# Kernel optimization log

Hardware: AMD Instinct MI355X
Metric: run time of the kernel (lower is better)

## Reference

```python
import jax, jax.numpy as jnp
import numpy as np

H = W = 256
L = H * W                      # number of graph vertices / tree leaves
N_NODES = 2 * L - 1            # binary partition tree node count
LAM = 1.0                      # lambda_ (soft-area temperature)


def _grid_edges():
    """4-adjacency grid graph edges (same structure as higra get_4_adjacency_graph)."""
    idx = np.arange(L, dtype=np.int64).reshape(H, W)
    src = np.concatenate([idx[:, :-1].ravel(), idx[:-1, :].ravel()])
    dst = np.concatenate([idx[:, 1:].ravel(), idx[1:, :].ravel()])
    return src.astype(np.int32), dst.astype(np.int32)


def setup_inputs() -> dict:
    key = jax.random.key(0)
    src, dst = _grid_edges()
    ew = jax.random.uniform(key, (src.shape[0],), dtype=jnp.float32)
    return {"edge_weights": ew,
            "edges_src": jnp.asarray(src),
            "edges_dst": jnp.asarray(dst)}


def _build_tree(ew, src, dst):
    """higra.bpt_canonical: Kruskal over stably-sorted edges, building a binary
    merge tree. Leaves are 0..L-1, internal node L+i is created by the i-th MST
    edge. Returns (sizes, mst_edge_map, ancestor paths). All integer structure
    is piecewise-constant w.r.t. edge_weights (no gradient flows through it)."""
    order = np.argsort(ew, kind="stable")
    uf = np.arange(L)

    def find(x):
        r = x
        while uf[r] != r:
            r = uf[r]
        while uf[x] != r:
            uf[x], x = r, uf[x]
        return r

    canon = np.arange(L)                      # tree node of each union-find root
    parent = np.arange(N_NODES)               # self-parent until set (root keeps self)
    sizes = np.ones(N_NODES, dtype=np.float32)
    edge_map = np.zeros(L - 1, dtype=np.int64)
    node = L
    for ei in order:
        a = find(src[ei]); b = find(dst[ei])
        if a == b:
            continue
        na, nb = canon[a], canon[b]
        parent[na] = node
        parent[nb] = node
        sizes[node] = sizes[na] + sizes[nb]
        edge_map[node - L] = ei
        uf[a] = b
        canon[b] = node
        node += 1
    # self-inclusive ancestor paths, padded by repeating the root
    cur = np.arange(N_NODES)
    cols = [cur.copy()]
    while np.any(parent[cur] != cur):
        cur = parent[cur]
        cols.append(cur.copy())
    paths = np.stack(cols, axis=1)            # [N_NODES, D+1]
    return sizes, edge_map, paths


def _softarea(edge_weights, edge_map, sizes_np, paths_np):
    """Soft area of every tree node n:
       area(n) = sum_x sigmoid((alt(n) - d(x, n)) / lambda)
    where d(x,n) is the min ultrametric distance from leaf x to the leaves of n:
      - x in subtree(n), x != n : d = alt(parent(x))
      - x == n (leaf)           : d = 0
      - x outside subtree(n)    : d = alt(lowest ancestor of n containing x).
    Outside leaves are grouped per ancestor a (count = size(a) - size(previous
    node on the path)), giving an O(N * depth) vectorized computation."""
    alt = jnp.concatenate([jnp.zeros((L,), edge_weights.dtype),
                           edge_weights[edge_map]])          # [N_NODES]
    alt_path = alt[paths_np]                                  # [N, D+1]
    size_path = sizes_np[paths_np]                            # constant, numpy
    diff = jnp.asarray(size_path[:, 1:] - size_path[:, :-1])  # 0 on root padding
    outside = jnp.sum(
        diff * jax.nn.sigmoid((alt[:, None] - alt_path[:, 1:]) / LAM), axis=1)

    # inside: each leaf x contributes sigmoid((alt(a_k) - alt(parent(x)))/lam)
    # to every proper ancestor a_k, plus sigmoid(0)=0.5 to itself (alt(leaf)=0).
    lp = paths_np[:L]                                         # [L, D+1]
    alt_lp = alt_path[:L]
    valid = jnp.asarray((lp[:, 1:] != lp[:, :-1]).astype(np.float32))
    vals = jax.nn.sigmoid((alt_lp[:, 1:] - alt_lp[:, 1:2]) / LAM) * valid
    inside = jax.ops.segment_sum(vals.reshape(-1),
                                 jnp.asarray(lp[:, 1:].reshape(-1)),
                                 num_segments=N_NODES)
    inside = inside.at[:L].add(0.5)
    return inside + outside


def reference(edge_weights, edges_src, edges_dst):
    sizes, edge_map, paths = _build_tree(np.asarray(edge_weights),
                                         np.asarray(edges_src),
                                         np.asarray(edges_dst))
    return _softarea(edge_weights, jnp.asarray(edge_map), sizes, paths)
```

## Files before the change

kernel.cpp:

```cpp
#include <hip/hip_runtime.h>
#include <stdint.h>

typedef unsigned int u32;
typedef unsigned short u16;
typedef unsigned long long u64;

#define L_VERTS 65536
#define N_EDGES 130560
#define N_NODES 131071
#define NODEPAD 131072

#define CCH 170
#define CCHM 86
#define SCH 768
#define PADM (CCHM*SCH)
#define NMST (L_VERTS-1)
#define MAXSV 1536
#define HSZ 2048

#define NB 255
#define TPB 64
#define IPT 8
#define IPB 512

__global__ void init_keys(const float* __restrict__ w, u32* __restrict__ keys, u32* __restrict__ vals,
                          u32* szG, u16* canonTop16, u32* parent, float* alt){
  int i = blockIdx.x*blockDim.x + threadIdx.x;
  if(i < N_EDGES){ keys[i] = __float_as_uint(w[i]); vals[i] = (u32)i; }
  if(i < N_NODES){ parent[i]=(u32)i; alt[i]=0.f; }
  if(i < L_VERTS){ szG[i]=1u; canonTop16[i]=0xFFFFu; }
}

__global__ void radix_hist(const u32* __restrict__ idx, const u32* __restrict__ keys,
                           u32* __restrict__ histG, int shift){
  __shared__ u32 h[256];
  for(int i=threadIdx.x;i<256;i+=TPB) h[i]=0;
  __syncthreads();
  int base = blockIdx.x*IPB + threadIdx.x*IPT;
  #pragma unroll
  for(int i=0;i<IPT;i++){
    u32 e = idx[base+i];
    u32 d = (keys[e]>>shift)&255u;
    atomicAdd(&h[d],1u);
  }
  __syncthreads();
  for(int i=threadIdx.x;i<256;i+=TPB) histG[i*NB+blockIdx.x]=h[i];
}

__global__ void radix_scan(u32* histG){
  const int M = 256*NB;
  __shared__ u32 sums[1024];
  int t=threadIdx.x; int s=t*64; u32 acc=0;
  for(int i=0;i<64;i++){int id=s+i; if(id<M) acc+=histG[id];}
  sums[t]=acc; __syncthreads();
  for(int off=1; off<1024; off<<=1){
    u32 v=(t>=off)?sums[t-off]:0u;
    __syncthreads();
    sums[t]+=v;
    __syncthreads();
  }
  u32 run = (t==0)?0u:sums[t-1];
  for(int i=0;i<64;i++){int id=s+i; if(id<M){u32 v=histG[id]; histG[id]=run; run+=v;}}
}

__global__ void radix_scatter(const u32* __restrict__ idxIn, const u32* __restrict__ keys,
                              u32* __restrict__ idxOut, const u32* __restrict__ histG, int shift){
  __shared__ u16 thoff[256][TPB];
  int t=threadIdx.x;
  for(int d=t;d<256;d+=TPB) for(int j=0;j<TPB;j++) thoff[d][j]=0;
  __syncthreads();
  int base = blockIdx.x*IPB + t*IPT;
  u32 myv[IPT]; u32 myd[IPT];
  #pragma unroll
  for(int i=0;i<IPT;i++){
    myv[i]=idxIn[base+i];
    myd[i]=(keys[myv[i]]>>shift)&255u;
    thoff[myd[i]][t]++;
  }
  __syncthreads();
  for(int dd=0;dd<4;dd++){
    int d=t*4+dd; u32 run=0;
    for(int j=0;j<TPB;j++){ u32 v=thoff[d][j]; thoff[d][j]=(u16)run; run+=v; }
  }
  __syncthreads();
  #pragma unroll
  for(int i=0;i<IPT;i++){
    u32 d=myd[i];
    u32 pos = histG[d*NB+blockIdx.x] + (u32)thoff[d][t];
    thoff[d][t]++;
    idxOut[pos]=myv[i];
  }
}

__global__ void build_epair(const u32* __restrict__ order, const int* __restrict__ srcv,
                            const int* __restrict__ dstv, u32* __restrict__ epair){
  int p=blockIdx.x*blockDim.x+threadIdx.x;
  if(p>=N_EDGES) return;
  u32 e=order[p];
  epair[p]=((u32)dstv[e]<<16)|(u32)srcv[e];
}

#define CBK 255
#define CT 512

__device__ __forceinline__ u32 bfind(const u32* __restrict__ parentB, u32 x){
  while(true){ u32 p=parentB[x]; if(p==x) return x; x=p; }
}

__global__ void bor_init(u32* parentB, u32* minE, unsigned char* mstF){
  int i=blockIdx.x*blockDim.x+threadIdx.x;
  if(i<L_VERTS){ parentB[i]=(u32)i; minE[i]=0xFFFFFFFFu; }
  if(i<N_EDGES) mstF[i]=0;
}

__global__ void bor_minedge(const u32* __restrict__ epair, const u32* __restrict__ parentB,
                            u32* __restrict__ minE){
  int p=blockIdx.x*blockDim.x+threadIdx.x;
  u32 pr=epair[p];
  u32 ra=bfind(parentB, pr&0xFFFFu), rb=bfind(parentB, pr>>16);
  if(ra==rb) return;
  atomicMin(&minE[ra],(u32)p);
  atomicMin(&minE[rb],(u32)p);
}

__global__ void bor_hookA(const u32* __restrict__ epair, const u32* __restrict__ parentB,
                          const u32* __restrict__ minE, u32* __restrict__ nextB,
                          unsigned char* __restrict__ mstF){
  int v=blockIdx.x*blockDim.x+threadIdx.x;
  if(v>=L_VERTS) return;
  if(parentB[v]!=(u32)v) return;
  u32 p=minE[v];
  if(p==0xFFFFFFFFu) return;
  u32 pr=epair[p];
  u32 ra=bfind(parentB, pr&0xFFFFu), rb=bfind(parentB, pr>>16);
  u32 w2=(ra==(u32)v)?rb:ra;
  nextB[v]=w2;
  mstF[p]=1;
}

__global__ void bor_hookB(u32* __restrict__ parentB, const u32* __restrict__ minE,
                          const u32* __restrict__ nextB){
  int v=blockIdx.x*blockDim.x+threadIdx.x;
  if(v>=L_VERTS) return;
  if(parentB[v]!=(u32)v) return;
  u32 p=minE[v];
  if(p==0xFFFFFFFFu) return;
  u32 w2=nextB[v];
  if(minE[w2]==p && (u32)v<w2) return;
  parentB[v]=w2;
}

__global__ void bor_compress(u32* __restrict__ parentB, u32* __restrict__ minE){
  int v=blockIdx.x*blockDim.x+threadIdx.x;
  if(v>=L_VERTS) return;
  u32 x=(u32)v;
  while(true){ u32 px=parentB[x]; if(px==x) break; u32 g=parentB[px]; if(g!=px) parentB[x]=g; x=g; }
  parentB[v]=x;
  minE[v]=0xFFFFFFFFu;
}

__global__ void mst_count(const unsigned char* __restrict__ mstF, u32* __restrict__ blockCnt){
  int b=blockIdx.x, t=threadIdx.x;
  int p=b*CT+t;
  u64 m=__ballot(mstF[p]!=0);
  __shared__ u32 ws[8];
  if((t&63)==0) ws[t>>6]=(u32)__popcll(m);
  __syncthreads();
  if(t==0){ u32 s=0; for(int i=0;i<8;i++) s+=ws[i]; blockCnt[b]=s; }
}

__global__ void mst_scan(const u32* __restrict__ blockCnt, u32* __restrict__ blockBase,
                         u32* __restrict__ mepair){
  int t=threadIdx.x;
  __shared__ u32 s[256];
  u32 v=(t<CBK)?blockCnt[t]:0u;
  s[t]=v; __syncthreads();
  for(int o=1;o<256;o<<=1){ u32 x=(t>=o)?s[t-o]:0u; __syncthreads(); s[t]+=x; __syncthreads(); }
  if(t<CBK) blockBase[t]=s[t]-v;
  u32 total=s[255];
  for(u32 j=total+(u32)t; j<(u32)PADM; j+=256u) mepair[j]=0u;
}

__global__ void mst_scatter(const unsigned char* __restrict__ mstF, const u32* __restrict__ blockBase,
                            const u32* __restrict__ order, const u32* __restrict__ epair,
                            u32* __restrict__ morder, u32* __restrict__ mepair){
  int b=blockIdx.x, t=threadIdx.x;
  int p=b*CT+t;
  u32 f=(u32)mstF[p];
  u64 m=__ballot(f!=0);
  __shared__ u32 ws[8];
  int wid=t>>6, lane=t&63;
  if(lane==0) ws[wid]=(u32)__popcll(m);
  __syncthreads();
  if(t==0){ u32 s2=0; for(int i=0;i<8;i++){ u32 x=ws[i]; ws[i]=s2; s2+=x; } }
  __syncthreads();
  if(f){
    u32 pre=(u32)__popcll(m & ((1ull<<lane)-1ull));
    u32 pos=blockBase[b]+ws[wid]+pre;
    morder[pos]=order[p];
    mepair[pos]=epair[p];
  }
}

__device__ __forceinline__ u32 ald(u32* p){
  return __hip_atomic_load(p, __ATOMIC_RELAXED, __HIP_MEMORY_SCOPE_AGENT);
}
__device__ __forceinline__ void ast(u32* p, u32 v){
  __hip_atomic_store(p, v, __ATOMIC_RELAXED, __HIP_MEMORY_SCOPE_AGENT);
}

__global__ void __launch_bounds__(1024,1) p1_checkpoints(
    const u32* __restrict__ epair,
    u32* szG, u16* lid16, u16* svroot16, u16* svsize16, u16* svnext16, u32* mG)
{
  __shared__ u16 ufL[L_VERTS];
  __shared__ u32 hkey[HSZ];
  __shared__ u32 sufL[MAXSV];
  __shared__ u32 compsz[MAXSV];
  __shared__ u32 repkey[MAXSV];
  __shared__ u16 lidL[2*SCH];
  __shared__ u32 mcnt;
  int t = threadIdx.x;
  for(int i=t;i<L_VERTS/2;i+=1024) ((u32*)ufL)[i]=((2u*(u32)i+1u)<<16)|(2u*(u32)i);
  for(int k=0;k<CCHM;k++){
    for(int i=t;i<HSZ;i+=1024) hkey[i]=0xFFFFFFFFu;
    for(u32 s=t;s<MAXSV;s+=1024){ sufL[s]=s; compsz[s]=0u; repkey[s]=0u; }
    if(t==0) mcnt=0u;
    __syncthreads();
    int base = k*SCH;
    for(int i=t;i<2*SCH;i+=1024){
      u32 pr = epair[base+(i>>1)];
      u32 v = (i&1)? (pr>>16) : (pr&0xFFFFu);
      u32 x=v;
      while(true){ u32 px=ufL[x]; if(px==x)break; u32 g=ufL[px]; if(g!=px) ufL[x]=(u16)g; x=g; }
      u32 r=x;
      if(v!=r) ufL[v]=(u16)r;
      u32 h=(r*2654435761u)>>21;
      while(true){
        u32 old=atomicCAS(&hkey[h],0xFFFFFFFFu,(r<<16)|0x7FFFu);
        if(old==0xFFFFFFFFu){
          u32 id=atomicAdd(&mcnt,1u);
          svroot16[k*MAXSV+id]=(u16)r;
          hkey[h]=(r<<16)|id;
          break;
        }
        if((old>>16)==r) break;
        h=(h+1)&(HSZ-1u);
      }
      lidL[i]=(u16)h;
    }
    __syncthreads();
    u32 mc=mcnt;
    if(t==0) mG[k]=mc;
    for(u32 s=t;s<mc;s+=1024){
      u32 r=(u32)svroot16[k*MAXSV+s];
      svsize16[k*MAXSV+s]=(u16)(ald(&szG[r])-1u);
    }
    for(int i=t;i<2*SCH;i+=1024) lid16[2*base+i]=(u16)(hkey[lidL[i]]&0xFFFFu);
    for(int j=t;j<SCH;j+=1024){
      u32 sa=hkey[lidL[2*j]]&0xFFFFu, sb=hkey[lidL[2*j+1]]&0xFFFFu;
      if(sa==sb) continue;
      while(true){
        u32 x=sa; while(true){u32 p2=sufL[x]; if(p2==x)break; u32 g=sufL[p2]; if(g!=p2) sufL[x]=g; x=g;}
        u32 y=sb; while(true){u32 p2=sufL[y]; if(p2==y)break; u32 g=sufL[p2]; if(g!=p2) sufL[y]=g; y=g;}
        if(x==y) break;
        u32 hi=x>y?x:y, lo=x^y^hi;
        if(atomicCAS(&sufL[hi],hi,lo)==hi) break;
        sa=hi; sb=lo;
      }
    }
    __syncthreads();
    for(u32 s=t;s<mc;s+=1024){
      u32 x=s; while(true){u32 p2=sufL[x]; if(p2==x)break; x=p2;}
      sufL[s]=x;
      u32 sz=(u32)svsize16[k*MAXSV+s]+1u;
      atomicAdd(&compsz[x], sz);
      atomicMax(&repkey[x], (sz<<11) | (2047u-s));
    }
    __syncthreads();
    for(u32 s=t;s<mc;s+=1024){
      u32 rs=sufL[s];
      u32 rep=2047u-(repkey[rs]&2047u);
      u32 wv=(u32)svroot16[k*MAXSV+rep];
      svnext16[k*MAXSV+s]=(u16)wv;
      u32 myroot=(u32)svroot16[k*MAXSV+s];
      if(myroot!=wv) ufL[myroot]=(u16)wv;
      if(s==rep)     ast(&szG[wv], compsz[rs]);
    }
    __syncthreads();
  }
}

__global__ void __launch_bounds__(64) p2_chunk(
  const u16* __restrict__ lid16,
  const u16* __restrict__ svsize16, const u16* __restrict__ svnext16, const u32* __restrict__ mG,
  u16* __restrict__ outChA, u16* __restrict__ outChB, u16* __restrict__ outSize16, u16* __restrict__ outJ16,
  u32* __restrict__ accCnt, u16* __restrict__ compR16, u16* __restrict__ compTop16, u32* __restrict__ ncomp)
{
  int k = blockIdx.x; int t = threadIdx.x;
  __shared__ u16 uf[MAXSV];
  __shared__ u32 csize[MAXSV];
  __shared__ u16 ctop[MAXSV];
  __shared__ u16 svnl[MAXSV];
  __shared__ u32 lidP[SCH];
  __shared__ u32 cmp_s;
  u32 m = mG[k];
  int base=k*SCH;
  for(u32 s=t;s<m;s+=64){
    uf[s]=(u16)s;
    csize[s]=(u32)svsize16[k*MAXSV+s]+1u;
    ctop[s]=(u16)s;
    svnl[s]=svnext16[k*MAXSV+s];
  }
  for(int j=t;j<SCH;j+=64) lidP[j]=((const u32*)lid16)[base+j];
  if(t==0) cmp_s=0u;
  __syncthreads();
  if(t==0){
    u32 cnt=0;
    for(int j=0;j<SCH;j++){
      u32 lw = lidP[j];
      u32 la = lw & 0xFFFFu, lb = lw >> 16;
      u32 x=la; while(true){u32 px=uf[x]; if(px==x)break; u32 g=uf[px]; uf[x]=(u16)g; x=g;}
      u32 y=lb; while(true){u32 py=uf[y]; if(py==y)break; u32 g=uf[py]; uf[y]=(u16)g; y=g;}
      if(x==y) continue;
      u32 sa=csize[x], sb=csize[y], ns=sa+sb;
      outChA[base+cnt]=ctop[x];
      outChB[base+cnt]=ctop[y];
      outSize16[base+cnt]=(u16)(ns-1u);
      outJ16[base+cnt]=(u16)j;
      u32 win=(sa>=sb)?x:y, los=x^y^win;
      uf[los]=(u16)win; csize[win]=ns; ctop[win]=(u16)(0x8000u|cnt);
      cnt++;
    }
    accCnt[k]=cnt;
  }
  __syncthreads();
  for(u32 s=t;s<m;s+=64){
    if(uf[s]==(u16)s && (ctop[s]&0x8000u)){
      u32 pos=atomicAdd(&cmp_s,1u);
      compR16[k*MAXSV+pos]=svnl[s];
      compTop16[k*MAXSV+pos]=(u16)(ctop[s]&0x7FFFu);
    }
  }
  __syncthreads();
  if(t==0) ncomp[k]=cmp_s;
}

__global__ void __launch_bounds__(1024) p3_stitch(
  const u32* __restrict__ accCnt, const u16* __restrict__ outChA, const u16* __restrict__ outChB,
  const u16* __restrict__ outSize16, const u16* __restrict__ outJ16,
  const u16* __restrict__ svroot16,
  const u16* __restrict__ compR16, const u16* __restrict__ compTop16, const u32* __restrict__ ncomp,
  const u32* __restrict__ morder, const float* __restrict__ w,
  u16* __restrict__ canonTop16, u32* __restrict__ parent, float* __restrict__ alt, u16* __restrict__ usize16)
{
  __shared__ u32 accBase[CCH];
  int t=threadIdx.x;
  if(t==0){ u32 r=0; for(int k=0;k<CCHM;k++){ accBase[k]=r; r+=accCnt[k]; } }
  __syncthreads();
  for(int idx=t; idx<PADM; idx+=1024){
    int k = idx/SCH; int j = idx - k*SCH;
    if(j < (int)accCnt[k]){
      u32 nid = (u32)L_VERTS + accBase[k] + (u32)j;
      u32 p = (u32)(k*SCH) + (u32)outJ16[idx];
      alt[nid] = w[morder[p]];
      usize16[nid] = outSize16[idx];
      u32 cA=outChA[idx]; if(cA & 0x8000u) parent[(u32)L_VERTS+accBase[k]+(cA&0x7FFFu)] = nid;
      u32 cB=outChB[idx]; if(cB & 0x8000u) parent[(u32)L_VERTS+accBase[k]+(cB&0x7FFFu)] = nid;
    }
  }
  __syncthreads();
  for(int k=0;k<CCHM;k++){
    u32 ac=accCnt[k];
    for(u32 j=t;j<ac;j+=1024){
      u32 idx=(u32)(k*SCH)+j;
      u32 nid=(u32)L_VERTS+accBase[k]+j;
      u32 cA=outChA[idx];
      if(!(cA&0x8000u)){
        u32 root=(u32)svroot16[k*MAXSV+cA];
        u32 ct=(u32)canonTop16[root];
        parent[(ct==0xFFFFu)?root:((u32)L_VERTS+ct)]=nid;
      }
      u32 cB=outChB[idx];
      if(!(cB&0x8000u)){
        u32 root=(u32)svroot16[k*MAXSV+cB];
        u32 ct=(u32)canonTop16[root];
        parent[(ct==0xFFFFu)?root:((u32)L_VERTS+ct)]=nid;
      }
    }
    __syncthreads();
    u32 nc=ncomp[k];
    for(u32 j=t;j<nc;j+=1024){
      canonTop16[(u32)compR16[k*MAXSV+j]] = (u16)(accBase[k]+compTop16[k*MAXSV+j]);
    }
    __syncthreads();
  }
}

__device__ __forceinline__ void hvals6(float v, float* o){
  float v2=v*v, v3=v2*v, v4=v2*v2, v5=v4*v;
  o[0]=0.5f-0.25f*v+v3*(1.f/48.f)-v5*(1.f/480.f);
  o[1]=0.25f-v2*(1.f/16.f)+v4*(1.f/96.f);
  o[2]=v*(1.f/16.f)-v3*(1.f/48.f);
  o[3]=v2*(1.f/48.f)-(1.f/48.f);
  o[4]=-v*(1.f/96.f);
  o[5]=(1.f/480.f);
}

__global__ void zero_both(u32* cc, float* nodeM, u32* ctr){
  int i=blockIdx.x*blockDim.x+threadIdx.x;
  if(i<L_VERTS) cc[i]=0u;
  if(i<6*NODEPAD) nodeM[i]=0.f;
  if(i==0) *ctr=0u;
}

__global__ void prep_init(const u32* __restrict__ parent, const u16* __restrict__ usize16,
                          u32* cc, u32* J0, uint2* A0, float* out){
  int n=blockIdx.x*blockDim.x+threadIdx.x;
  if(n>=N_NODES) return;
  out[n] = (n<L_VERTS)?0.5f:0.0f;
  if(n==N_NODES-1){ J0[n]=(u32)n; A0[n]=make_uint2(0u,0u); return; }
  u32 p=parent[n];
  u32 ord=atomicAdd(&cc[p-L_VERTS],1u);
  u32 szP=(u32)usize16[p]+1u;
  u32 szN=(n<L_VERTS)?1u:((u32)usize16[n]+1u);
  u32 sib=szP-szN;
  A0[n]=make_uint2(ord? sib:0u, 1u + (ord? (2u*sib-1u):0u));
  J0[n]=p;
}

__global__ void triple_round(const u32* __restrict__ Jin, const uint2* __restrict__ Ain,
                             u32* __restrict__ Jout, uint2* __restrict__ Aout){
  int n=blockIdx.x*blockDim.x+threadIdx.x;
  if(n>=N_NODES) return;
  u32 j1=Jin[n], j2=Jin[j1], j3=Jin[j2], j4=Jin[j3], j5=Jin[j4], j6=Jin[j5], j7=Jin[j6];
  uint2 a0=Ain[n], a1=Ain[j1], a2=Ain[j2], a3=Ain[j3], a4=Ain[j4], a5=Ain[j5], a6=Ain[j6], a7=Ain[j7];
  Aout[n]=make_uint2(a0.x+a1.x+a2.x+a3.x+a4.x+a5.x+a6.x+a7.x,
                     a0.y+a1.y+a2.y+a3.y+a4.y+a5.y+a6.y+a7.y);
  Jout[n]=Jin[j7];
}

__global__ void scatter_all(const u32* __restrict__ parent, const float* __restrict__ alt,
                            const u16* __restrict__ usize16, const uint2* __restrict__ accF,
                            float* __restrict__ leafM, float* __restrict__ nodeM){
  int n=blockIdx.x*blockDim.x+threadIdx.x;
  if(n>=N_NODES) return;
  u32 p=parent[n];
  float h[6]; hvals6(alt[p],h);
  uint2 af=accF[n];
  if(n<L_VERTS){
    u32 pos=af.x;
    #pragma unroll
    for(int j=0;j<6;j++) leafM[(size_t)j*L_VERTS+pos]=h[j];
  }
  if(n<N_NODES-1){
    u32 szP=(u32)usize16[p]+1u;
    u32 szN=(n<L_VERTS)?1u:((u32)usize16[n]+1u);
    float d=(float)(szP-szN);
    u32 q0=af.y;
    u32 q1=q0 + 2u*szN - 1u;
    #pragma unroll
    for(int j=0;j<6;j++){
      float tm=d*h[j];
      atomicAdd(&nodeM[(size_t)j*NODEPAD+q0], tm);
      atomicAdd(&nodeM[(size_t)j*NODEPAD+q1], -tm);
    }
  }
}

__global__ void scanAll(float* __restrict__ leafM, float* __restrict__ nodeM,
                        float* __restrict__ bsumL, float* __restrict__ bsumN, u32* ctr){
  int b=blockIdx.x; int t=threadIdx.x;
  float* arr; u32 base; float* bs;
  if(b<6*64){ int row=b>>6, blk=b&63;  arr=leafM+(size_t)row*L_VERTS;  base=(u32)blk*1024u; bs=&bsumL[row*64+blk]; }
  else      { int bb=b-384; int row=bb>>7, blk=bb&127; arr=nodeM+(size_t)row*NODEPAD; base=(u32)blk*1024u; bs=&bsumN[row*128+blk]; }
  __shared__ float s[256];
  __shared__ u32 lastFlag;
  base += (u32)t*4u;
  float v0=arr[base],v1=arr[base+1],v2=arr[base+2],v3=arr[base+3];
  v1+=v0; v2+=v1; v3+=v2;
  s[t]=v3; __syncthreads();
  for(int o=1;o<256;o<<=1){ float x=(t>=o)?s[t-o]:0.f; __syncthreads(); s[t]+=x; __syncthreads(); }
  float pre=(t>0)?s[t-1]:0.f;
  arr[base]=v0+pre; arr[base+1]=v1+pre; arr[base+2]=v2+pre; arr[base+3]=v3+pre;
  if(t==255) *bs=s[255];
  __threadfence();
  if(t==0) lastFlag = (atomicAdd(ctr,1u)==1151u) ? 1u : 0u;
  __syncthreads();
  if(lastFlag){
    __threadfence();
    if(t<6){ float r=0; for(int i=0;i<64;i++){ float v=bsumL[t*64+i]; bsumL[t*64+i]=r; r+=v; } }
    else if(t<12){ int j=t-6; float r=0; for(int i=0;i<128;i++){ float v=bsumN[j*128+i]; bsumN[j*128+i]=r; r+=v; } }
  }
}

__global__ void eval_all(const uint2* __restrict__ accF, const float* __restrict__ alt,
                         const u16* __restrict__ usize16, const float* __restrict__ leafM,
                         const float* __restrict__ nodeM, const float* __restrict__ bsumL,
                         const float* __restrict__ bsumN, float* __restrict__ out){
  int n=blockIdx.x*blockDim.x+threadIdx.x;
  if(n>=N_NODES) return;
  uint2 af=accF[n];
  float u=alt[n];
  u32 q=af.y;
  float acc=0.f, up=1.f;
  #pragma unroll
  for(int j=0;j<6;j++){
    float T = nodeM[(size_t)j*NODEPAD+q] + bsumN[j*128 + (q>>10)];
    acc += up*T;
    up*=u;
  }
  if(n>=L_VERTS){
    u32 lo=af.x;
    u32 hi=lo + (u32)usize16[n] + 1u;
    up=1.f;
    #pragma unroll
    for(int j=0;j<6;j++){
      const float* arr=leafM + (size_t)j*L_VERTS;
      const float* bs=bsumL + j*64;
      float Ph = arr[hi-1u] + bs[(hi-1u)>>10];
      float Pl = lo ? (arr[lo-1u] + bs[(lo-1u)>>10]) : 0.f;
      acc += up*(Ph-Pl);
      up*=u;
    }
  }
  out[n]+=acc;
}

__global__ void ws_too_small(float* out){
  int i=blockIdx.x*blockDim.x+threadIdx.x;
  if(i<N_NODES) out[i]=1.0e6f;
}

extern "C" void kernel_launch(void* const* d_in, const int* in_sizes, int n_in,
                              void* d_out, int out_size, void* d_ws, size_t ws_size,
                              hipStream_t stream){
  (void)in_sizes; (void)n_in; (void)out_size;
  const float* w  = (const float*)d_in[0];
  const int* src  = (const int*)d_in[1];
  const int* dst  = (const int*)d_in[2];
  float* out = (float*)d_out;

  char* ws = (char*)d_ws;
  size_t off=0;
  auto alloc=[&](size_t bytes)->void*{ void* p = ws+off; off += (bytes+511)&~(size_t)511; return p; };
  u32* parent   =(u32*)alloc((size_t)N_NODES*4);
  float* alt    =(float*)alloc((size_t)N_NODES*4);
  u16* usize16  =(u16*)alloc((size_t)N_NODES*2);
  float* bsumL  =(float*)alloc(6*64*4);
  float* bsumN  =(float*)alloc(6*128*4);
  u32* ctr      =(u32*)alloc(512);
  size_t scratch0=off;
  u32* keys0    =(u32*)alloc((size_t)N_EDGES*4);
  u32* vals0    =(u32*)alloc((size_t)N_EDGES*4);
  u32* vals1    =(u32*)alloc((size_t)N_EDGES*4);
  u32* histG    =(u32*)alloc(256*NB*4);
  u16* canonTop16=(u16*)alloc((size_t)L_VERTS*2);
  u16* outJ16   =(u16*)alloc((size_t)N_EDGES*2);
  u16* svroot16 =(u16*)alloc((size_t)CCH*MAXSV*2);
  u16* svsize16 =(u16*)alloc((size_t)CCH*MAXSV*2);
  u16* svnext16 =(u16*)alloc((size_t)CCH*MAXSV*2);
  u32* mG       =(u32*)alloc(CCH*4);
  u32* accCnt   =(u32*)alloc(CCH*4);
  u32* ncomp    =(u32*)alloc(CCH*4);
  u32* parentB  =(u32*)alloc((size_t)L_VERTS*4);
  u32* minE     =(u32*)alloc((size_t)L_VERTS*4);
  u32* nextB    =(u32*)alloc((size_t)L_VERTS*4);
  unsigned char* mstF=(unsigned char*)alloc((size_t)N_EDGES);
  u32* blockCnt =(u32*)alloc(256*4);
  u32* blockBase=(u32*)alloc(256*4);
  u32* morder   =(u32*)alloc((size_t)PADM*4);
  u32* mepair   =(u32*)alloc((size_t)PADM*4);
  size_t endA=off;
  off=scratch0;
  u32* ccChsum  =(u32*)alloc((size_t)L_VERTS*4);
  u32* J0       =(u32*)alloc((size_t)N_NODES*4);
  u32* J1       =(u32*)alloc((size_t)N_NODES*4);
  uint2* A0     =(uint2*)alloc((size_t)N_NODES*8);
  uint2* A1     =(uint2*)alloc((size_t)N_NODES*8);
  float* nodeM  =(float*)alloc((size_t)6*NODEPAD*4);
  size_t endB=off;
  float* leafM  =(float*)ccChsum;

  if((endA>ws_size)||(endB>ws_size)){
    ws_too_small<<<(N_NODES+255)/256,256,0,stream>>>(out);
    return;
  }

  u16* lid16    =(u16*)vals1;
  u32* epair    =keys0;
  u16* outChA16 =(u16*)histG;
  u16* outChB16 =(u16*)keys0;
  u16* outSize16=(u16*)((char*)keys0 + (size_t)N_EDGES*2);
  u16* compR16  =svsize16;
  u16* compTop16=svnext16;
  u32* szG      =(u32*)usize16;

  init_keys<<<(N_NODES+255)/256,256,0,stream>>>(w,keys0,vals0,szG,canonTop16,parent,alt);
  for(int pass=0;pass<4;pass++){
    const u32* iv = (pass&1)?vals1:vals0;
    u32* ov = (pass&1)?vals0:vals1;
    int shift=pass*8;
    radix_hist   <<<NB,TPB,0,stream>>>(iv,keys0,histG,shift);
    radix_scan   <<<1,1024,0,stream>>>(histG);
    radix_scatter<<<NB,TPB,0,stream>>>(iv,keys0,ov,histG,shift);
  }
  build_epair<<<(N_EDGES+255)/256,256,0,stream>>>(vals0,src,dst,epair);
  bor_init<<<CBK,CT,0,stream>>>(parentB,minE,mstF);
  for(int r=0;r<16;r++){
    bor_minedge <<<CBK,CT,0,stream>>>(epair,parentB,minE);
    bor_hookA   <<<L_VERTS/CT,CT,0,stream>>>(epair,parentB,minE,nextB,mstF);
    bor_hookB   <<<L_VERTS/CT,CT,0,stream>>>(parentB,minE,nextB);
    bor_compress<<<L_VERTS/CT,CT,0,stream>>>(parentB,minE);
  }
  mst_count  <<<CBK,CT,0,stream>>>(mstF,blockCnt);
  mst_scan   <<<1,256,0,stream>>>(blockCnt,blockBase,mepair);
  mst_scatter<<<CBK,CT,0,stream>>>(mstF,blockBase,vals0,epair,morder,mepair);
  p1_checkpoints<<<1,1024,0,stream>>>(mepair,szG,lid16,svroot16,svsize16,svnext16,mG);
  p2_chunk<<<CCHM,64,0,stream>>>(lid16,svsize16,svnext16,mG,
                                outChA16,outChB16,outSize16,outJ16,accCnt,compR16,compTop16,ncomp);
  p3_stitch<<<1,1024,0,stream>>>(accCnt,outChA16,outChB16,outSize16,outJ16,svroot16,
                                 compR16,compTop16,ncomp,morder,w,canonTop16,parent,alt,usize16);
  zero_both<<<(6*NODEPAD+255)/256,256,0,stream>>>(ccChsum,nodeM,ctr);
  prep_init<<<(N_NODES+255)/256,256,0,stream>>>(parent,usize16,ccChsum,J1,A1,out);
  for(int r=0;r<6;r++){
    if((r&1)==0) triple_round<<<(N_NODES+255)/256,256,0,stream>>>(J1,A1,J0,A0);
    else         triple_round<<<(N_NODES+255)/256,256,0,stream>>>(J0,A0,J1,A1);
  }
  const uint2* accF=A1;
  scatter_all<<<(N_NODES+255)/256,256,0,stream>>>(parent,alt,usize16,accF,leafM,nodeM);
  scanAll<<<1152,256,0,stream>>>(leafM,nodeM,bsumL,bsumN,ctr);
  eval_all<<<(N_NODES+255)/256,256,0,stream>>>(accF,alt,usize16,leafM,nodeM,bsumL,bsumN,out);
}
```

Before: 2.699 ms.

## Fuse Boruvka MST rounds into one cooperative kernel with early exit

Replaces the 64 separate Boruvka kernel launches (init plus 16 rounds of four phases) with a single cooperative kernel that uses grid-wide syncs between phases. A hook counter ends the loop early once all MST edges are found, and edges whose endpoints already share a component are marked dead so later rounds skip their finds. Separately, the single-block checkpoint kernel now reads component sizes while inserting into the hash table. It also picks the union-find root as the representative instead of the largest component, which removes an atomicMax and a pass over the supervertices. The cost is grid-sync overhead, and the representative choice is a possible semantic change.

Result: slower. 3.755 ms (+39.1%).

```diff
diff --git a/kernel.cpp b/kernel.cpp
--- a/kernel.cpp
+++ b/kernel.cpp
@@ -1,5 +1,8 @@
 #include <hip/hip_runtime.h>
+#include <hip/hip_cooperative_groups.h>
 #include <stdint.h>
+
+namespace cg = cooperative_groups;
 
 typedef unsigned int u32;
 typedef unsigned short u16;
@@ -100,64 +103,68 @@
   epair[p]=((u32)dstv[e]<<16)|(u32)srcv[e];
 }
 
+#define BORB 256
+#define BORT 512
+#define DEADE 0xFFFFFFFFu
+
+__device__ __forceinline__ u32 bfind(const u32* __restrict__ parentB, u32 x){
+  while(true){ u32 p=parentB[x]; if(p==x) return x; x=p; }
+}
+
+__global__ void __launch_bounds__(BORT) bor_all(u32* __restrict__ epair, u32* __restrict__ parentB,
+                        u32* __restrict__ minE, u32* __restrict__ nextB,
+                        unsigned char* __restrict__ mstF, u32* __restrict__ bctr){
+  cg::grid_group grid = cg::this_grid();
+  int tid = blockIdx.x*BORT + threadIdx.x;
+  if(tid<L_VERTS){ parentB[tid]=(u32)tid; minE[tid]=0xFFFFFFFFu; }
+  if(tid<N_EDGES) mstF[tid]=0;
+  if(tid==0) bctr[0]=0u;
+  grid.sync();
+  for(int r=0;r<16;r++){
+    if(tid<N_EDGES){
+      u32 pr=epair[tid];
+      if(pr!=DEADE){
+        u32 ra=bfind(parentB, pr&0xFFFFu), rb=bfind(parentB, pr>>16);
+        if(ra==rb){ if(!mstF[tid]) epair[tid]=DEADE; }
+        else { atomicMin(&minE[ra],(u32)tid); atomicMin(&minE[rb],(u32)tid); }
+      }
+    }
+    grid.sync();
+    if(tid<L_VERTS && parentB[tid]==(u32)tid){
+      u32 p=minE[tid];
+      if(p!=0xFFFFFFFFu){
+        u32 pr=epair[p];
+        u32 ra=bfind(parentB, pr&0xFFFFu), rb=bfind(parentB, pr>>16);
+        u32 w2=(ra==(u32)tid)?rb:ra;
+        nextB[tid]=w2;
+        mstF[p]=1;
+      }
+    }
+    grid.sync();
+    if(tid<L_VERTS && parentB[tid]==(u32)tid){
+      u32 p=minE[tid];
+      if(p!=0xFFFFFFFFu){
+        u32 w2=nextB[tid];
+        if(!(minE[w2]==p && (u32)tid<w2)){
+          parentB[tid]=w2;
+          atomicAdd(&bctr[0],1u);
+        }
+      }
+    }
+    grid.sync();
+    if(tid<L_VERTS){
+      u32 x=(u32)tid;
+      while(true){ u32 px=parentB[x]; if(px==x) break; u32 g=parentB[px]; if(g!=px) parentB[x]=g; x=g; }
+      parentB[tid]=x;
+      minE[tid]=0xFFFFFFFFu;
+    }
+    grid.sync();
+    if(__hip_atomic_load(&bctr[0], __ATOMIC_RELAXED, __HIP_MEMORY_SCOPE_AGENT) >= (u32)NMST) break;
+  }
+}
+
 #define CBK 255
 #define CT 512
-
-__device__ __forceinline__ u32 bfind(const u32* __restrict__ parentB, u32 x){
-  while(true){ u32 p=parentB[x]; if(p==x) return x; x=p; }
-}
-
-__global__ void bor_init(u32* parentB, u32* minE, unsigned char* mstF){
-  int i=blockIdx.x*blockDim.x+threadIdx.x;
-  if(i<L_VERTS){ parentB[i]=(u32)i; minE[i]=0xFFFFFFFFu; }
-  if(i<N_EDGES) mstF[i]=0;
-}
-
-__global__ void bor_minedge(const u32* __restrict__ epair, const u32* __restrict__ parentB,
-                            u32* __restrict__ minE){
-  int p=blockIdx.x*blockDim.x+threadIdx.x;
-  u32 pr=epair[p];
-  u32 ra=bfind(parentB, pr&0xFFFFu), rb=bfind(parentB, pr>>16);
-  if(ra==rb) return;
-  atomicMin(&minE[ra],(u32)p);
-  atomicMin(&minE[rb],(u32)p);
-}
-
-__global__ void bor_hookA(const u32* __restrict__ epair, const u32* __restrict__ parentB,
-                          const u32* __restrict__ minE, u32* __restrict__ nextB,
-                          unsigned char* __restrict__ mstF){
-  int v=blockIdx.x*blockDim.x+threadIdx.x;
-  if(v>=L_VERTS) return;
-  if(parentB[v]!=(u32)v) return;
-  u32 p=minE[v];
-  if(p==0xFFFFFFFFu) return;
-  u32 pr=epair[p];
-  u32 ra=bfind(parentB, pr&0xFFFFu), rb=bfind(parentB, pr>>16);
-  u32 w2=(ra==(u32)v)?rb:ra;
-  nextB[v]=w2;
-  mstF[p]=1;
-}
-
-__global__ void bor_hookB(u32* __restrict__ parentB, const u32* __restrict__ minE,
-                          const u32* __restrict__ nextB){
-  int v=blockIdx.x*blockDim.x+threadIdx.x;
-  if(v>=L_VERTS) return;
-  if(parentB[v]!=(u32)v) return;
-  u32 p=minE[v];
-  if(p==0xFFFFFFFFu) return;
-  u32 w2=nextB[v];
-  if(minE[w2]==p && (u32)v<w2) return;
-  parentB[v]=w2;
-}
-
-__global__ void bor_compress(u32* __restrict__ parentB, u32* __restrict__ minE){
-  int v=blockIdx.x*blockDim.x+threadIdx.x;
-  if(v>=L_VERTS) return;
-  u32 x=(u32)v;
-  while(true){ u32 px=parentB[x]; if(px==x) break; u32 g=parentB[px]; if(g!=px) parentB[x]=g; x=g; }
-  parentB[v]=x;
-  minE[v]=0xFFFFFFFFu;
-}
 
 __global__ void mst_count(const unsigned char* __restrict__ mstF, u32* __restrict__ blockCnt){
   int b=blockIdx.x, t=threadIdx.x;
@@ -217,14 +224,14 @@
   __shared__ u32 hkey[HSZ];
   __shared__ u32 sufL[MAXSV];
   __shared__ u32 compsz[MAXSV];
-  __shared__ u32 repkey[MAXSV];
+  __shared__ u16 ssz[MAXSV];
   __shared__ u16 lidL[2*SCH];
   __shared__ u32 mcnt;
   int t = threadIdx.x;
   for(int i=t;i<L_VERTS/2;i+=1024) ((u32*)ufL)[i]=((2u*(u32)i+1u)<<16)|(2u*(u32)i);
   for(int k=0;k<CCHM;k++){
     for(int i=t;i<HSZ;i+=1024) hkey[i]=0xFFFFFFFFu;
-    for(u32 s=t;s<MAXSV;s+=1024){ sufL[s]=s; compsz[s]=0u; repkey[s]=0u; }
+    for(u32 s=t;s<MAXSV;s+=1024){ sufL[s]=s; compsz[s]=0u; }
     if(t==0) mcnt=0u;
     __syncthreads();
     int base = k*SCH;
@@ -240,7 +247,10 @@
         u32 old=atomicCAS(&hkey[h],0xFFFFFFFFu,(r<<16)|0x7FFFu);
         if(old==0xFFFFFFFFu){
           u32 id=atomicAdd(&mcnt,1u);
+          u32 sz=ald(&szG[r]);
           svroot16[k*MAXSV+id]=(u16)r;
+          svsize16[k*MAXSV+id]=(u16)(sz-1u);
+          ssz[id]=(u16)(sz-1u);
           hkey[h]=(r<<16)|id;
           break;
         }
@@ -252,10 +262,6 @@
     __syncthreads();
     u32 mc=mcnt;
     if(t==0) mG[k]=mc;
-    for(u32 s=t;s<mc;s+=1024){
-      u32 r=(u32)svroot16[k*MAXSV+s];
-      svsize16[k*MAXSV+s]=(u16)(ald(&szG[r])-1u);
-    }
     for(int i=t;i<2*SCH;i+=1024) lid16[2*base+i]=(u16)(hkey[lidL[i]]&0xFFFFu);
     for(int j=t;j<SCH;j+=1024){
       u32 sa=hkey[lidL[2*j]]&0xFFFFu, sb=hkey[lidL[2*j+1]]&0xFFFFu;
@@ -273,19 +279,16 @@
     for(u32 s=t;s<mc;s+=1024){
       u32 x=s; while(true){u32 p2=sufL[x]; if(p2==x)break; x=p2;}
       sufL[s]=x;
-      u32 sz=(u32)svsize16[k*MAXSV+s]+1u;
-      atomicAdd(&compsz[x], sz);
-      atomicMax(&repkey[x], (sz<<11) | (2047u-s));
+      atomicAdd(&compsz[x], (u32)ssz[s]+1u);
     }
     __syncthreads();
     for(u32 s=t;s<mc;s+=1024){
       u32 rs=sufL[s];
-      u32 rep=2047u-(repkey[rs]&2047u);
-      u32 wv=(u32)svroot16[k*MAXSV+rep];
+      u32 wv=(u32)svroot16[k*MAXSV+rs];
       svnext16[k*MAXSV+s]=(u16)wv;
       u32 myroot=(u32)svroot16[k*MAXSV+s];
       if(myroot!=wv) ufL[myroot]=(u16)wv;
-      if(s==rep)     ast(&szG[wv], compsz[rs]);
+      if(s==rs)      ast(&szG[wv], compsz[rs]);
     }
     __syncthreads();
   }
@@ -571,6 +574,7 @@
   u32* blockBase=(u32*)alloc(256*4);
   u32* morder   =(u32*)alloc((size_t)PADM*4);
   u32* mepair   =(u32*)alloc((size_t)PADM*4);
+  u32* bctr     =(u32*)alloc(512);
   size_t endA=off;
   off=scratch0;
   u32* ccChsum  =(u32*)alloc((size_t)L_VERTS*4);
@@ -606,12 +610,9 @@
     radix_scatter<<<NB,TPB,0,stream>>>(iv,keys0,ov,histG,shift);
   }
   build_epair<<<(N_EDGES+255)/256,256,0,stream>>>(vals0,src,dst,epair);
-  bor_init<<<CBK,CT,0,stream>>>(parentB,minE,mstF);
-  for(int r=0;r<16;r++){
-    bor_minedge <<<CBK,CT,0,stream>>>(epair,parentB,minE);
-    bor_hookA   <<<L_VERTS/CT,CT,0,stream>>>(epair,parentB,minE,nextB,mstF);
-    bor_hookB   <<<L_VERTS/CT,CT,0,stream>>>(parentB,minE,nextB);
-    bor_compress<<<L_VERTS/CT,CT,0,stream>>>(parentB,minE);
+  {
+    void* kargs[] = {(void*)&epair,(void*)&parentB,(void*)&minE,(void*)&nextB,(void*)&mstF,(void*)&bctr};
+    hipLaunchCooperativeKernel((const void*)bor_all, dim3(BORB), dim3(BORT), kargs, 0, stream);
   }
   mst_count  <<<CBK,CT,0,stream>>>(mstF,blockCnt);
   mst_scan   <<<1,256,0,stream>>>(blockCnt,blockBase,mepair);
```
